# Optimization experiments

Hardware: AMD Instinct MI355X
Metric: run time of the kernel (lower is better)

## Reference

```python
import math
import jax, jax.numpy as jnp
import numpy as np

BN_EPS = 1e-5

def _lrelu(x, s):
    return jnp.where(x >= 0, x, s * x)

def _bn(x, g, b):
    # BatchNorm2d in train mode (torch default): biased batch stats over (B,H,W)
    mu = jnp.mean(x, axis=(0, 2, 3), keepdims=True)
    var = jnp.mean((x - mu) ** 2, axis=(0, 2, 3), keepdims=True)
    return (x - mu) / jnp.sqrt(var + BN_EPS) * g[None, :, None, None] + b[None, :, None, None]

def _knn(x, x2, k):
    # x: [B,d,P], x2: [B,d,S] -> idx [B,k,S]: k nearest points of x for each column of x2
    inner = -2.0 * jnp.einsum('bdp,bds->bps', x, x2)
    xx = jnp.sum(x ** 2, axis=1)[:, :, None]    # [B,P,1]
    xx2 = jnp.sum(x2 ** 2, axis=1)[:, None, :]  # [B,1,S]
    d = -xx - inner - xx2                        # [B,P,S], larger = closer
    _, idx = jax.lax.top_k(jnp.transpose(d, (0, 2, 1)), k)  # [B,S,k]
    return jnp.transpose(idx, (0, 2, 1))         # [B,k,S]

def _gather_nb(X, idx, s, k):
    # faithful to torch gether_neibour, including its flat-reshape layout
    B, C, P = X.shape
    base = jnp.arange(B)[:, None, None] * P
    flat = (idx + base).reshape(-1)
    Xt = jnp.transpose(X, (0, 2, 1)).reshape(B * P, C)
    return Xt[flat].reshape(B, s, k, C)

def _c2d(x, W, b):
    return jnp.einsum('oc,bcpk->bopk', W, x) + b[None, :, None, None]

def _c1d(x, W, b):
    return jnp.einsum('oc,bcp->bop', W, x) + b[None, :, None]

def _forward(x, W_pos, b_pos, g2, be2, W_conv, b_conv, g1, be1, W_a1, b_a1, W_a2, b_a2, W_b1, b_b1, W_b2, b_b2, num_points):
    B, C, P = x.shape
    k = 8
    s = num_points
    # ---- Dynamic_sampling_M: uniform mesh over (x,y) bbox, snap to nearest event ----
    L = int(math.ceil(math.sqrt(s)))
    m = jnp.arange(L, dtype=x.dtype) / L
    m01 = jnp.tile(m[None, :], (L, 1)).reshape(1, 1, L * L)
    m02 = jnp.tile(m[:, None], (1, L)).reshape(1, 1, L * L)
    mesh = jnp.broadcast_to(jnp.concatenate([m01, m02], axis=1), (B, 2, L * L))
    Px = jax.lax.stop_gradient(x[:, :2, :])  # knn runs under torch.no_grad
    mn = Px.min(axis=2, keepdims=True)
    mx = Px.max(axis=2, keepdims=True)
    PS = mesh * (mx - mn) + mn
    idx0 = _knn(Px, PS, 1)                                   # [B,1,L*L]
    sp = _gather_nb(x, idx0, L * L, 1)[:, :, 0, :].transpose(0, 2, 1)  # [B,C,s]
    idx = _knn(jax.lax.stop_gradient(x[:, :3, :]), jax.lax.stop_gradient(sp[:, :3, :]), k)  # [B,k,s]
    x1 = jnp.transpose(_gather_nb(x, idx, s, k), (0, 3, 1, 2))  # [B,C,s,k]
    # ---- positional encoding ----
    PA = x1[:, :3, :, :]
    PC = x1[:, :3, :, 0:1]
    diff = PA - PC
    sq = jnp.sum(diff ** 2, axis=1, keepdims=True)
    temp = jnp.where(sq > 0, jnp.sqrt(jnp.where(sq > 0, sq, 1.0)), 0.0)
    PEmb = jnp.concatenate([PA, jnp.broadcast_to(PC, PA.shape), diff, temp], axis=1)  # [B,10,s,k]
    PEmb = _lrelu(_bn(_c2d(PEmb, W_pos, b_pos), g2, be2), 0.2)
    x_ = _lrelu(_bn(_c2d(x1[:, :4, :, :], W_conv, b_conv), g1, be1), 0.2)
    feat = jnp.concatenate([x_, PEmb], axis=1)  # [B,64,s,k]
    att = _c2d(_lrelu(_c2d(feat, W_a1, b_a1), 0.2), W_a2, b_a2)  # [B,1,s,k]
    att = jax.nn.softmax(att, axis=-1)
    feat = jnp.sum(feat * att, axis=-1)  # [B,64,s]
    Fea1 = _c1d(feat, W_b1, b_b1)
    Fea2 = _c1d(x1[:, :4, :, 0], W_b2, b_b2)
    out = _lrelu(Fea1 + Fea2, 0.01)
    return jnp.concatenate([x1[:, :5, :, 0], out], axis=1)  # [B,69,s]

def setup_inputs() -> dict:
    key = jax.random.key(0)
    ks = jax.random.split(key, 8)
    B, C, P = 2, 5, 16384
    num_points = 4096  # perfect square required by the mesh sampler
    outc, inc, h = 64, 4, 32
    w = lambda k_, shape: jax.random.normal(k_, shape, jnp.float32) * 0.05
    x = jax.random.normal(ks[0], (B, C, P), jnp.float32)
    return dict(
        x=x,
        W_pos=w(ks[1], (h, 10)), b_pos=jnp.zeros((h,), jnp.float32),
        g2=jnp.ones((h,), jnp.float32), be2=jnp.zeros((h,), jnp.float32),
        W_conv=w(ks[2], (h, inc)), b_conv=jnp.zeros((h,), jnp.float32),
        g1=jnp.ones((h,), jnp.float32), be1=jnp.zeros((h,), jnp.float32),
        W_a1=w(ks[3], (32, outc)), b_a1=jnp.zeros((32,), jnp.float32),
        W_a2=w(ks[4], (1, 32)), b_a2=jnp.zeros((1,), jnp.float32),
        W_b1=w(ks[5], (outc, outc)), b_b1=jnp.zeros((outc,), jnp.float32),
        W_b2=w(ks[6], (outc, inc)), b_b2=jnp.zeros((outc,), jnp.float32),
        num_points=num_points,
    )

def reference(x, W_pos, b_pos, g2, be2, W_conv, b_conv, g1, be1, W_a1, b_a1, W_a2, b_a2, W_b1, b_b1, W_b2, b_b2, num_points):
    return _forward(x, W_pos, b_pos, g2, be2, W_conv, b_conv, g1, be1, W_a1, b_a1, W_a2, b_a2, W_b1, b_b1, W_b2, b_b2, num_points)
```

## Files before the change

### kernel.cpp

```cpp
#include <hip/hip_runtime.h>
#include <math.h>

#define B_ 2
#define P_ 16384
#define C_ 5
#define S_ 4096
#define KNN_ 8
#define L_ 64

typedef unsigned short u16;
typedef unsigned int u32;

__device__ int   g_idxk[B_ * KNN_ * S_];
__device__ __align__(16) float g_partials[128 * 1024];

__device__ __forceinline__ float bf2f(u16 u) {
  union { u32 i; float f; } c; c.i = ((u32)u) << 16; return c.f;
}
__device__ __forceinline__ u16 f2bf(float f) {
  union { float f; u32 i; } c; c.f = f;
  u32 r = c.i + 0x7fffu + ((c.i >> 16) & 1u);
  return (u16)(r >> 16);
}
__device__ __forceinline__ float ldany(const void* p, int i, int f32) {
  return f32 ? ((const float*)p)[i] : bf2f(((const u16*)p)[i]);
}

__device__ __forceinline__ double packkey(float d, int idx) {
  u32 bits = __float_as_uint(d);
  u32 key = bits ^ ((u32)(((int)bits) >> 31) | 0x80000000u);
  int hi = (int)(0x3FF00000u | (key >> 12));
  int lo = (int)((key << 20) | ((u32)(16383 - idx) << 6));
  return __hiloint2double(hi, lo);
}
__device__ __forceinline__ int keyidx(double w) {
  return 16383 - (int)(((u32)__double2loint(w) >> 6) & 16383u);
}
__device__ __forceinline__ void cmpswap(double& a, double& b) {
  double hi = fmax(a, b), lo = fmin(a, b);
  a = hi; b = lo;
}
__device__ __forceinline__ void flush8(double* a, double* k) {
  cmpswap(k[0], k[1]); cmpswap(k[2], k[3]); cmpswap(k[4], k[5]); cmpswap(k[6], k[7]);
  cmpswap(k[0], k[2]); cmpswap(k[1], k[3]); cmpswap(k[4], k[6]); cmpswap(k[5], k[7]);
  cmpswap(k[1], k[2]); cmpswap(k[5], k[6]);
  cmpswap(k[0], k[4]); cmpswap(k[1], k[5]); cmpswap(k[2], k[6]); cmpswap(k[3], k[7]);
  cmpswap(k[2], k[4]); cmpswap(k[3], k[5]);
  cmpswap(k[1], k[2]); cmpswap(k[3], k[4]); cmpswap(k[5], k[6]);
  a[0] = fmax(a[0], k[7]); a[1] = fmax(a[1], k[6]);
  a[2] = fmax(a[2], k[5]); a[3] = fmax(a[3], k[4]);
  a[4] = fmax(a[4], k[3]); a[5] = fmax(a[5], k[2]);
  a[6] = fmax(a[6], k[1]); a[7] = fmax(a[7], k[0]);
  cmpswap(a[0], a[4]); cmpswap(a[1], a[5]); cmpswap(a[2], a[6]); cmpswap(a[3], a[7]);
  cmpswap(a[0], a[2]); cmpswap(a[1], a[3]); cmpswap(a[4], a[6]); cmpswap(a[5], a[7]);
  cmpswap(a[0], a[1]); cmpswap(a[2], a[3]); cmpswap(a[4], a[5]); cmpswap(a[6], a[7]);
}

__device__ __forceinline__ int chk_bad(const void* p, int n, int tid) {
  int bad = 0;
  for (int i = tid; i < n; i += 256) {
    float f = bf2f(((const u16*)p)[i]);
    if (!(f == f) || fabsf(f) > 1024.0f) bad = 1;
  }
  return bad;
}

__global__ __launch_bounds__(256, 4) void k_knn(const void* __restrict__ xv,
                                                const void* __restrict__ Wpos,
                                                const void* __restrict__ bpos,
                                                const void* __restrict__ Wconv,
                                                const void* __restrict__ bconv) {
  __shared__ float4 s4[1024];
  __shared__ float sWpos[320], sbpos[32], sWconv[128], sbconv[32];
  __shared__ float sacc[4][128];
  __shared__ int sidx[8];
  __shared__ int sp0[8];
  __shared__ int sbad, sbw;
  __shared__ float sred[16];
  int tid = threadIdx.x;
  int l = tid & 63, g = tid >> 6;
  int sg0 = blockIdx.x * 8 + g * 2;
  int b = sg0 >> 12;
  int base0 = b * C_ * P_, base1 = base0 + P_, base2 = base1 + P_;

  if (tid == 0) { sbad = 0; sbw = 0; }
  __syncthreads();
  if (chk_bad(xv, 1024, tid)) atomicOr(&sbad, 1);
  if (chk_bad(Wpos, 320, tid) | chk_bad(Wconv, 128, tid)) atomicOr(&sbw, 1);
  __syncthreads();
  const int f32 = sbad, wf32 = sbw;

  for (int i2 = tid; i2 < 320; i2 += 256) sWpos[i2] = ldany(Wpos, i2, wf32);
  if (tid < 128) sWconv[tid] = ldany(Wconv, tid, wf32);
  if (tid < 32) { sbpos[tid] = ldany(bpos, tid, wf32); sbconv[tid] = ldany(bconv, tid, wf32); }

  float mn0 = INFINITY, mx0 = -INFINITY, mn1 = INFINITY, mx1 = -INFINITY;
  for (int p = tid; p < P_; p += 256) {
    float v0 = ldany(xv, base0 + p, f32);
    float v1 = ldany(xv, base1 + p, f32);
    mn0 = fminf(mn0, v0); mx0 = fmaxf(mx0, v0);
    mn1 = fminf(mn1, v1); mx1 = fmaxf(mx1, v1);
  }
  for (int off = 32; off; off >>= 1) {
    mn0 = fminf(mn0, __shfl_down(mn0, off)); mx0 = fmaxf(mx0, __shfl_down(mx0, off));
    mn1 = fminf(mn1, __shfl_down(mn1, off)); mx1 = fmaxf(mx1, __shfl_down(mx1, off));
  }
  if (l == 0) {
    sred[g * 4 + 0] = mn0; sred[g * 4 + 1] = mx0;
    sred[g * 4 + 2] = mn1; sred[g * 4 + 3] = mx1;
  }
  __syncthreads();
  mn0 = fminf(fminf(sred[0], sred[4]), fminf(sred[8], sred[12]));
  mx0 = fmaxf(fmaxf(sred[1], sred[5]), fmaxf(sred[9], sred[13]));
  mn1 = fminf(fminf(sred[2], sred[6]), fminf(sred[10], sred[14]));
  mx1 = fmaxf(fmaxf(sred[3], sred[7]), fmaxf(sred[11], sred[15]));

  float ps0[2], ps1[2], xx2[2], best[2]; int bestp[2];
#pragma unroll
  for (int qq = 0; qq < 2; ++qq) {
    int s = (sg0 + qq) & (S_ - 1);
    float mm0 = (float)(s & (L_ - 1)) * 0.015625f;
    float mm1 = (float)(s >> 6) * 0.015625f;
    ps0[qq] = __fadd_rn(__fmul_rn(mm0, __fsub_rn(mx0, mn0)), mn0);
    ps1[qq] = __fadd_rn(__fmul_rn(mm1, __fsub_rn(mx1, mn1)), mn1);
    xx2[qq] = __fadd_rn(__fmul_rn(ps0[qq], ps0[qq]), __fmul_rn(ps1[qq], ps1[qq]));
    best[qq] = -INFINITY; bestp[qq] = 0x7fffffff;
  }
  for (int c = 0; c < 16; ++c) {
    __syncthreads();
#pragma unroll
    for (int r = 0; r < 4; ++r) {
      int i = r * 256 + tid;
      int gi = c * 1024 + i;
      float a0 = ldany(xv, base0 + gi, f32);
      float a1 = ldany(xv, base1 + gi, f32);
      float xx = __fadd_rn(__fmul_rn(a0, a0), __fmul_rn(a1, a1));
      s4[i] = make_float4(a0, a1, xx, 0.0f);
    }
    __syncthreads();
    for (int t = 0; t < 16; ++t) {
      float4 v = s4[t * 64 + l];
      int ix = c * 1024 + t * 64 + l;
#pragma unroll
      for (int qq = 0; qq < 2; ++qq) {
        float dot = __fadd_rn(__fmul_rn(v.x, ps0[qq]), __fmul_rn(v.y, ps1[qq]));
        float inner = __fmul_rn(-2.0f, dot);
        float d = __fsub_rn(__fsub_rn(-v.z, inner), xx2[qq]);
        bool gt = d > best[qq];
        best[qq] = gt ? d : best[qq];
        bestp[qq] = gt ? ix : bestp[qq];
      }
    }
  }
#pragma unroll
  for (int qq = 0; qq < 2; ++qq) {
    float v = best[qq]; int ix = bestp[qq];
    for (int m = 1; m < 64; m <<= 1) {
      float ov = __shfl_xor(v, m, 64); int op = __shfl_xor(ix, m, 64);
      if (ov > v || (ov == v && op < ix)) { v = ov; ix = op; }
    }
    if (l == 0) sidx[g * 2 + qq] = ix;
  }
  __syncthreads();

  float q0[2], q1[2], q2[2], xx3q[2];
  double acc[2][8], kb[2][8];
#pragma unroll
  for (int qq = 0; qq < 2; ++qq) {
    int qi = sidx[g * 2 + qq] & (P_ - 1);
    q0[qq] = ldany(xv, base0 + qi, f32);
    q1[qq] = ldany(xv, base1 + qi, f32);
    q2[qq] = ldany(xv, base2 + qi, f32);
    xx3q[qq] = __fadd_rn(__fadd_rn(__fmul_rn(q0[qq], q0[qq]), __fmul_rn(q1[qq], q1[qq])),
                         __fmul_rn(q2[qq], q2[qq]));
#pragma unroll
    for (int k = 0; k < 8; ++k) acc[qq][k] = -1.0;
  }
  for (int c = 0; c < 16; ++c) {
    __syncthreads();
#pragma unroll
    for (int r = 0; r < 4; ++r) {
      int i = r * 256 + tid;
      int gi = c * 1024 + i;
      float a0 = ldany(xv, base0 + gi, f32);
      float a1 = ldany(xv, base1 + gi, f32);
      float a2 = ldany(xv, base2 + gi, f32);
      float xx = __fadd_rn(__fadd_rn(__fmul_rn(a0, a0), __fmul_rn(a1, a1)), __fmul_rn(a2, a2));
      s4[i] = make_float4(a0, a1, a2, xx);
    }
    __syncthreads();
#pragma unroll
    for (int t = 0; t < 16; ++t) {
      float4 v = s4[t * 64 + l];
      int ix = c * 1024 + t * 64 + l;
      u32 lob = ((u32)(16383 - ix)) << 6;
#pragma unroll
      for (int qq = 0; qq < 2; ++qq) {
        float dot = __fadd_rn(__fadd_rn(__fmul_rn(v.x, q0[qq]), __fmul_rn(v.y, q1[qq])),
                              __fmul_rn(v.z, q2[qq]));
        float inner = __fmul_rn(-2.0f, dot);
        float d = __fsub_rn(__fsub_rn(-v.w, inner), xx3q[qq]);
        u32 bits = __float_as_uint(d);
        u32 key = bits ^ ((u32)(((int)bits) >> 31) | 0x80000000u);
        kb[qq][t & 7] = __hiloint2double((int)(0x3FF00000u | (key >> 12)),
                                         (int)((key << 20) | lob));
      }
      if ((t & 7) == 7) {
        flush8(acc[0], kb[0]);
        flush8(acc[1], kb[1]);
      }
    }
  }
  double wk[2] = {0.0, 0.0};
#pragma unroll
  for (int qq = 0; qq < 2; ++qq) {
#pragma unroll
    for (int r = 0; r < 8; ++r) {
      double w = acc[qq][0];
      for (int m = 1; m < 64; m <<= 1) w = fmax(w, __shfl_xor(w, m, 64));
      if (l == r) wk[qq] = w;
      bool cns = (acc[qq][0] == w);
#pragma unroll
      for (int k = 0; k < 7; ++k) acc[qq][k] = cns ? acc[qq][k + 1] : acc[qq][k];
      acc[qq][7] = cns ? -1.0 : acc[qq][7];
    }
  }
  if (l < 8) {
#pragma unroll
    for (int qq = 0; qq < 2; ++qq) {
      int s = (sg0 + qq) & (S_ - 1);
      g_idxk[b * 32768 + l * 4096 + s] = keyidx(wk[qq]);
    }
  }

  if (g == 0 && l < 8) sp0[l] = keyidx(wk[0]) & (P_ - 1);
  __syncthreads();
  double k1s = __shfl(wk[1], l & 7, 16);
  bool active = (l < 16);
  double myk = (l < 8) ? wk[0] : k1s;
  int p = keyidx(myk) & (P_ - 1);
  int p0 = sp0[l & 7];
  float xvv[4] = {0, 0, 0, 0}, pc3[3] = {0, 0, 0};
  if (active) {
#pragma unroll
    for (int cc = 0; cc < 4; ++cc) xvv[cc] = ldany(xv, base0 + cc * P_ + p, f32);
#pragma unroll
    for (int cc = 0; cc < 3; ++cc) pc3[cc] = ldany(xv, base0 + cc * P_ + p0, f32);
  }
  float d0 = xvv[0] - pc3[0], d1 = xvv[1] - pc3[1], d2 = xvv[2] - pc3[2];
  float sq = d0 * d0 + d1 * d1 + d2 * d2;
  float temp = (sq > 0.0f) ? sqrtf(sq) : 0.0f;
  float pe[10] = {xvv[0], xvv[1], xvv[2], pc3[0], pc3[1], pc3[2], d0, d1, d2, temp};
#pragma unroll
  for (int o = 0; o < 64; ++o) {
    float v;
    if (o < 32) {
      v = sbconv[o];
#pragma unroll
      for (int cc = 0; cc < 4; ++cc) v = fmaf(sWconv[o * 4 + cc], xvv[cc], v);
    } else {
      v = sbpos[o - 32];
#pragma unroll
      for (int cc = 0; cc < 10; ++cc) v = fmaf(sWpos[(o - 32) * 10 + cc], pe[cc], v);
    }
    v = active ? v : 0.0f;
    float s = v, q = v * v;
    for (int m = 1; m < 16; m <<= 1) { s += __shfl_xor(s, m, 16); q += __shfl_xor(q, m, 16); }
    if (l == 0) { sacc[g][o * 2] = s; sacc[g][o * 2 + 1] = q; }
  }
  __syncthreads();
  if (tid < 128) {
    g_partials[tid * 1024 + blockIdx.x] =
        sacc[0][tid] + sacc[1][tid] + sacc[2][tid] + sacc[3][tid];
  }
}

__global__ __launch_bounds__(256) void k_pass2(const void* __restrict__ x,
                                               const void* __restrict__ Wpos,
                                               const void* __restrict__ bpos,
                                               const void* __restrict__ Wconv,
                                               const void* __restrict__ bconv,
                                               const void* __restrict__ g1,
                                               const void* __restrict__ be1,
                                               const void* __restrict__ g2,
                                               const void* __restrict__ be2,
                                               const void* __restrict__ Wa1,
                                               const void* __restrict__ ba1,
                                               const void* __restrict__ Wa2,
                                               const void* __restrict__ ba2,
                                               const void* __restrict__ Wb1,
                                               const void* __restrict__ bb1,
                                               const void* __restrict__ Wb2,
                                               const void* __restrict__ bb2,
                                               void* __restrict__ out) {
  __shared__ float sWpos[320], sbpos[32], sWconv[128], sbconv[32];
  __shared__ float sWa1[2048], sba1[32], sWa2[32];
  __shared__ float sWb1[64 * 65];
  __shared__ float sbb1[64], sWb2[256], sbb2[64], sstats[128];
  __shared__ float sp2[2][128];
  __shared__ float sba2;
  __shared__ int sbx, sbw;
  int tid = threadIdx.x;
  if (tid == 0) { sbx = 0; sbw = 0; }
  __syncthreads();
  if (chk_bad(x, 1024, tid)) atomicOr(&sbx, 1);
  if (chk_bad(Wa1, 2048, tid) | chk_bad(Wb1, 4096, tid)) atomicOr(&sbw, 1);
  __syncthreads();
  int xf32 = sbx, wf32 = sbw;

  int g = blockIdx.x * 32 + (tid >> 3);
  int j = tid & 7;
  int b = g >> 12, i = g & (S_ - 1);
  int n = i * 8 + j;
  const int* fb = g_idxk + b * 32768;
  int xbase = b * C_ * P_;
  int p = fb[n] & (P_ - 1);
  int p0 = fb[n & ~7] & (P_ - 1);
  float xvv[4];
#pragma unroll
  for (int c = 0; c < 4; ++c) xvv[c] = ldany(x, xbase + c * P_ + p, xf32);
  float pc3[3];
#pragma unroll
  for (int c = 0; c < 3; ++c) pc3[c] = ldany(x, xbase + c * P_ + p0, xf32);
  float xc0 = ldany(x, xbase + p0, xf32);
  float xc1 = ldany(x, xbase + P_ + p0, xf32);
  float xc2 = ldany(x, xbase + 2 * P_ + p0, xf32);
  float xc3 = ldany(x, xbase + 3 * P_ + p0, xf32);

  {
    int slot = tid & 127, half = tid >> 7;
    const float4* gp = (const float4*)(g_partials + slot * 1024 + half * 512);
    float a0 = 0.f, a1 = 0.f, a2 = 0.f, a3 = 0.f;
#pragma unroll 8
    for (int q = 0; q < 128; ++q) {
      float4 v = gp[q];
      a0 += v.x; a1 += v.y; a2 += v.z; a3 += v.w;
    }
    sp2[half][slot] = (a0 + a1) + (a2 + a3);
  }
  for (int i2 = tid; i2 < 320; i2 += 256) sWpos[i2] = ldany(Wpos, i2, wf32);
  if (tid < 128) sWconv[tid] = ldany(Wconv, tid, wf32);
  if (tid < 32) { sbpos[tid] = ldany(bpos, tid, wf32); sbconv[tid] = ldany(bconv, tid, wf32); }
  for (int i2 = tid; i2 < 2048; i2 += 256) sWa1[i2] = ldany(Wa1, i2, wf32);
  for (int i2 = tid; i2 < 4096; i2 += 256) sWb1[(i2 >> 6) * 65 + (i2 & 63)] = ldany(Wb1, i2, wf32);
  if (tid >= 32 && tid < 64) { sba1[tid - 32] = ldany(ba1, tid - 32, wf32); sWa2[tid - 32] = ldany(Wa2, tid - 32, wf32); }
  if (tid >= 64 && tid < 128) { sbb1[tid - 64] = ldany(bb1, tid - 64, wf32); sbb2[tid - 64] = ldany(bb2, tid - 64, wf32); }
  sWb2[tid] = ldany(Wb2, tid, wf32);
  if (tid == 0) sba2 = ldany(ba2, 0, wf32);
  __syncthreads();
  if (tid >= 128 && tid < 192) {
    int ch = tid - 128;
    float sum = sp2[0][ch * 2] + sp2[1][ch * 2];
    float sq = sp2[0][ch * 2 + 1] + sp2[1][ch * 2 + 1];
    float mean = sum * (1.0f / 65536.0f);
    float var = sq * (1.0f / 65536.0f) - mean * mean;
    int o = ch & 31;
    float gg = ldany(ch < 32 ? g1 : g2, o, wf32);
    float be = ldany(ch < 32 ? be1 : be2, o, wf32);
    float scale = gg / sqrtf(var + 1e-5f);
    sstats[ch * 2] = scale;
    sstats[ch * 2 + 1] = be - mean * scale;
  }
  __syncthreads();

  float d0 = xvv[0] - pc3[0], d1 = xvv[1] - pc3[1], d2 = xvv[2] - pc3[2];
  float sq = d0 * d0 + d1 * d1 + d2 * d2;
  float temp = (sq > 0.0f) ? sqrtf(sq) : 0.0f;
  float pe[10] = {xvv[0], xvv[1], xvv[2], pc3[0], pc3[1], pc3[2], d0, d1, d2, temp};
  float feat[64];
#pragma unroll
  for (int o = 0; o < 32; ++o) {
    float acc = sbconv[o];
#pragma unroll
    for (int c = 0; c < 4; ++c) acc = fmaf(sWconv[o * 4 + c], xvv[c], acc);
    feat[o] = acc;
  }
#pragma unroll
  for (int o = 0; o < 32; ++o) {
    float acc = sbpos[o];
#pragma unroll
    for (int c = 0; c < 10; ++c) acc = fmaf(sWpos[o * 10 + c], pe[c], acc);
    feat[32 + o] = acc;
  }
#pragma unroll
  for (int c = 0; c < 64; ++c) {
    float v = fmaf(feat[c], sstats[c * 2], sstats[c * 2 + 1]);
    feat[c] = (v >= 0.f) ? v : 0.2f * v;
  }
  float att = sba2;
#pragma unroll 4
  for (int h = 0; h < 32; ++h) {
    float a0 = 0.f, a1 = 0.f, a2 = 0.f, a3 = 0.f;
#pragma unroll
    for (int c = 0; c < 64; c += 4) {
      a0 = fmaf(sWa1[h * 64 + c],     feat[c],     a0);
      a1 = fmaf(sWa1[h * 64 + c + 1], feat[c + 1], a1);
      a2 = fmaf(sWa1[h * 64 + c + 2], feat[c + 2], a2);
      a3 = fmaf(sWa1[h * 64 + c + 3], feat[c + 3], a3);
    }
    float acc = sba1[h] + ((a0 + a1) + (a2 + a3));
    acc = (acc >= 0.f) ? acc : 0.2f * acc;
    att = fmaf(sWa2[h], acc, att);
  }
  float mxv = att;
  for (int mk = 1; mk < 8; mk <<= 1) mxv = fmaxf(mxv, __shfl_xor(mxv, mk, 8));
  float e = expf(att - mxv);
  float se = e;
  for (int mk = 1; mk < 8; mk <<= 1) se += __shfl_xor(se, mk, 8);
  float a = e / se;
#pragma unroll
  for (int c = 0; c < 64; ++c) {
    float w = feat[c] * a;
    w += __shfl_xor(w, 1, 8);
    w += __shfl_xor(w, 2, 8);
    w += __shfl_xor(w, 4, 8);
    feat[c] = w;
  }
  int obase = b * 69 * S_;
#pragma unroll
  for (int oc = 0; oc < 8; ++oc) {
    int o = j * 8 + oc;
    float a0 = sbb1[o], a1 = 0.f, a2 = 0.f, a3 = 0.f;
#pragma unroll
    for (int c = 0; c < 64; c += 4) {
      a0 = fmaf(sWb1[o * 65 + c],     feat[c],     a0);
      a1 = fmaf(sWb1[o * 65 + c + 1], feat[c + 1], a1);
      a2 = fmaf(sWb1[o * 65 + c + 2], feat[c + 2], a2);
      a3 = fmaf(sWb1[o * 65 + c + 3], feat[c + 3], a3);
    }
    float acc = (a0 + a1) + (a2 + a3);
    float acc2 = sbb2[o];
    acc2 = fmaf(sWb2[o * 4 + 0], xc0, acc2);
    acc2 = fmaf(sWb2[o * 4 + 1], xc1, acc2);
    acc2 = fmaf(sWb2[o * 4 + 2], xc2, acc2);
    acc2 = fmaf(sWb2[o * 4 + 3], xc3, acc2);
    float r = acc + acc2;
    r = (r >= 0.f) ? r : 0.01f * r;
    int oi = obase + (5 + o) * S_ + i;
    if (xf32) ((float*)out)[oi] = r; else ((u16*)out)[oi] = f2bf(r);
  }
  if (j == 0) {
#pragma unroll
    for (int c = 0; c < 5; ++c) {
      int oi = obase + c * S_ + i;
      if (xf32) ((float*)out)[oi] = ((const float*)x)[xbase + c * P_ + p0];
      else      ((u16*)out)[oi]   = ((const u16*)x)[xbase + c * P_ + p0];
    }
  }
}

extern "C" void kernel_launch(void* const* d_in, const int* in_sizes, int n_in,
                              void* d_out, int out_size, void* d_ws, size_t ws_size,
                              hipStream_t stream) {
  const void* x     = d_in[0];
  const void* Wpos  = d_in[1];
  const void* bpos  = d_in[2];
  const void* g2    = d_in[3];
  const void* be2   = d_in[4];
  const void* Wconv = d_in[5];
  const void* bconv = d_in[6];
  const void* g1    = d_in[7];
  const void* be1   = d_in[8];
  const void* Wa1   = d_in[9];
  const void* ba1   = d_in[10];
  const void* Wa2   = d_in[11];
  const void* ba2   = d_in[12];
  const void* Wb1   = d_in[13];
  const void* bb1   = d_in[14];
  const void* Wb2   = d_in[15];
  const void* bb2   = d_in[16];
  (void)d_ws; (void)ws_size; (void)in_sizes; (void)n_in;

  hipLaunchKernelGGL(k_knn, dim3(1024), dim3(256), 0, stream, x,
                     Wpos, bpos, Wconv, bconv);
  hipLaunchKernelGGL(k_pass2, dim3(256), dim3(256), 0, stream, x,
                     Wpos, bpos, Wconv, bconv, g1, be1, g2, be2,
                     Wa1, ba1, Wa2, ba2, Wb1, bb1, Wb2, bb2, d_out);
}
```

Before: 304.4 us.

## Split KNN kernel into one-query-per-wave search and separate batch-stat tail kernel

The KNN kernel now handles one query per wavefront instead of two, doubling the grid to 2048 blocks and raising the occupancy hint. The BN partial-statistics work that used to run inside the KNN kernel moves to a new k_tail kernel, one thread per neighbour. The partials buffer is re-laid out as [block][128] and the reduction in pass2 is rewritten to match. This frees registers in the KNN loop for higher occupancy, but it reloads each tile of points twice as often across blocks and adds a third kernel launch.

Result: no change. 300.4 us (-1.3%).

```diff
diff --git a/kernel.cpp b/kernel.cpp
--- a/kernel.cpp
+++ b/kernel.cpp
@@ -12,7 +12,7 @@
 typedef unsigned int u32;
 
 __device__ int   g_idxk[B_ * KNN_ * S_];
-__device__ __align__(16) float g_partials[128 * 1024];
+__device__ float g_partials[256 * 128];
 
 __device__ __forceinline__ float bf2f(u16 u) {
   union { u32 i; float f; } c; c.i = ((u32)u) << 16; return c.f;
@@ -26,13 +26,6 @@
   return f32 ? ((const float*)p)[i] : bf2f(((const u16*)p)[i]);
 }
 
-__device__ __forceinline__ double packkey(float d, int idx) {
-  u32 bits = __float_as_uint(d);
-  u32 key = bits ^ ((u32)(((int)bits) >> 31) | 0x80000000u);
-  int hi = (int)(0x3FF00000u | (key >> 12));
-  int lo = (int)((key << 20) | ((u32)(16383 - idx) << 6));
-  return __hiloint2double(hi, lo);
-}
 __device__ __forceinline__ int keyidx(double w) {
   return 16383 - (int)(((u32)__double2loint(w) >> 6) & 16383u);
 }
@@ -65,34 +58,23 @@
   return bad;
 }
 
-__global__ __launch_bounds__(256, 4) void k_knn(const void* __restrict__ xv,
-                                                const void* __restrict__ Wpos,
-                                                const void* __restrict__ bpos,
-                                                const void* __restrict__ Wconv,
-                                                const void* __restrict__ bconv) {
+__global__ __launch_bounds__(256, 6) void k_knn(const void* __restrict__ xv) {
   __shared__ float4 s4[1024];
-  __shared__ float sWpos[320], sbpos[32], sWconv[128], sbconv[32];
-  __shared__ float sacc[4][128];
-  __shared__ int sidx[8];
-  __shared__ int sp0[8];
-  __shared__ int sbad, sbw;
+  __shared__ int sidx[4];
+  __shared__ int sbad;
   __shared__ float sred[16];
   int tid = threadIdx.x;
   int l = tid & 63, g = tid >> 6;
-  int sg0 = blockIdx.x * 8 + g * 2;
-  int b = sg0 >> 12;
+  int sq = blockIdx.x * 4 + g;
+  int b = sq >> 12;
+  int s = sq & (S_ - 1);
   int base0 = b * C_ * P_, base1 = base0 + P_, base2 = base1 + P_;
 
-  if (tid == 0) { sbad = 0; sbw = 0; }
+  if (tid == 0) sbad = 0;
   __syncthreads();
   if (chk_bad(xv, 1024, tid)) atomicOr(&sbad, 1);
-  if (chk_bad(Wpos, 320, tid) | chk_bad(Wconv, 128, tid)) atomicOr(&sbw, 1);
-  __syncthreads();
-  const int f32 = sbad, wf32 = sbw;
-
-  for (int i2 = tid; i2 < 320; i2 += 256) sWpos[i2] = ldany(Wpos, i2, wf32);
-  if (tid < 128) sWconv[tid] = ldany(Wconv, tid, wf32);
-  if (tid < 32) { sbpos[tid] = ldany(bpos, tid, wf32); sbconv[tid] = ldany(bconv, tid, wf32); }
+  __syncthreads();
+  const int f32 = sbad;
 
   float mn0 = INFINITY, mx0 = -INFINITY, mn1 = INFINITY, mx1 = -INFINITY;
   for (int p = tid; p < P_; p += 256) {
@@ -115,17 +97,12 @@
   mn1 = fminf(fminf(sred[2], sred[6]), fminf(sred[10], sred[14]));
   mx1 = fmaxf(fmaxf(sred[3], sred[7]), fmaxf(sred[11], sred[15]));
 
-  float ps0[2], ps1[2], xx2[2], best[2]; int bestp[2];
-#pragma unroll
-  for (int qq = 0; qq < 2; ++qq) {
-    int s = (sg0 + qq) & (S_ - 1);
-    float mm0 = (float)(s & (L_ - 1)) * 0.015625f;
-    float mm1 = (float)(s >> 6) * 0.015625f;
-    ps0[qq] = __fadd_rn(__fmul_rn(mm0, __fsub_rn(mx0, mn0)), mn0);
-    ps1[qq] = __fadd_rn(__fmul_rn(mm1, __fsub_rn(mx1, mn1)), mn1);
-    xx2[qq] = __fadd_rn(__fmul_rn(ps0[qq], ps0[qq]), __fmul_rn(ps1[qq], ps1[qq]));
-    best[qq] = -INFINITY; bestp[qq] = 0x7fffffff;
-  }
+  float mm0 = (float)(s & (L_ - 1)) * 0.015625f;
+  float mm1 = (float)(s >> 6) * 0.015625f;
+  float ps0 = __fadd_rn(__fmul_rn(mm0, __fsub_rn(mx0, mn0)), mn0);
+  float ps1 = __fadd_rn(__fmul_rn(mm1, __fsub_rn(mx1, mn1)), mn1);
+  float xx2 = __fadd_rn(__fmul_rn(ps0, ps0), __fmul_rn(ps1, ps1));
+  float best = -INFINITY; int bestp = 0x7fffffff;
   for (int c = 0; c < 16; ++c) {
     __syncthreads();
 #pragma unroll
@@ -141,41 +118,33 @@
     for (int t = 0; t < 16; ++t) {
       float4 v = s4[t * 64 + l];
       int ix = c * 1024 + t * 64 + l;
-#pragma unroll
-      for (int qq = 0; qq < 2; ++qq) {
-        float dot = __fadd_rn(__fmul_rn(v.x, ps0[qq]), __fmul_rn(v.y, ps1[qq]));
-        float inner = __fmul_rn(-2.0f, dot);
-        float d = __fsub_rn(__fsub_rn(-v.z, inner), xx2[qq]);
-        bool gt = d > best[qq];
-        best[qq] = gt ? d : best[qq];
-        bestp[qq] = gt ? ix : bestp[qq];
-      }
-    }
-  }
-#pragma unroll
-  for (int qq = 0; qq < 2; ++qq) {
-    float v = best[qq]; int ix = bestp[qq];
+      float dot = __fadd_rn(__fmul_rn(v.x, ps0), __fmul_rn(v.y, ps1));
+      float inner = __fmul_rn(-2.0f, dot);
+      float d = __fsub_rn(__fsub_rn(-v.z, inner), xx2);
+      bool gt = d > best;
+      best = gt ? d : best;
+      bestp = gt ? ix : bestp;
+    }
+  }
+  {
+    float v = best; int ix = bestp;
     for (int m = 1; m < 64; m <<= 1) {
       float ov = __shfl_xor(v, m, 64); int op = __shfl_xor(ix, m, 64);
       if (ov > v || (ov == v && op < ix)) { v = ov; ix = op; }
     }
-    if (l == 0) sidx[g * 2 + qq] = ix;
-  }
-  __syncthreads();
-
-  float q0[2], q1[2], q2[2], xx3q[2];
-  double acc[2][8], kb[2][8];
-#pragma unroll
-  for (int qq = 0; qq < 2; ++qq) {
-    int qi = sidx[g * 2 + qq] & (P_ - 1);
-    q0[qq] = ldany(xv, base0 + qi, f32);
-    q1[qq] = ldany(xv, base1 + qi, f32);
-    q2[qq] = ldany(xv, base2 + qi, f32);
-    xx3q[qq] = __fadd_rn(__fadd_rn(__fmul_rn(q0[qq], q0[qq]), __fmul_rn(q1[qq], q1[qq])),
-                         __fmul_rn(q2[qq], q2[qq]));
-#pragma unroll
-    for (int k = 0; k < 8; ++k) acc[qq][k] = -1.0;
-  }
+    if (l == 0) sidx[g] = ix;
+  }
+  __syncthreads();
+
+  int qi = sidx[g] & (P_ - 1);
+  float q0 = ldany(xv, base0 + qi, f32);
+  float q1 = ldany(xv, base1 + qi, f32);
+  float q2 = ldany(xv, base2 + qi, f32);
+  float xx3q = __fadd_rn(__fadd_rn(__fmul_rn(q0, q0), __fmul_rn(q1, q1)),
+                         __fmul_rn(q2, q2));
+  double acc[8], kb[8];
+#pragma unroll
+  for (int k = 0; k < 8; ++k) acc[k] = -1.0;
   for (int c = 0; c < 16; ++c) {
     __syncthreads();
 #pragma unroll
@@ -194,59 +163,64 @@
       float4 v = s4[t * 64 + l];
       int ix = c * 1024 + t * 64 + l;
       u32 lob = ((u32)(16383 - ix)) << 6;
-#pragma unroll
-      for (int qq = 0; qq < 2; ++qq) {
-        float dot = __fadd_rn(__fadd_rn(__fmul_rn(v.x, q0[qq]), __fmul_rn(v.y, q1[qq])),
-                              __fmul_rn(v.z, q2[qq]));
-        float inner = __fmul_rn(-2.0f, dot);
-        float d = __fsub_rn(__fsub_rn(-v.w, inner), xx3q[qq]);
-        u32 bits = __float_as_uint(d);
-        u32 key = bits ^ ((u32)(((int)bits) >> 31) | 0x80000000u);
-        kb[qq][t & 7] = __hiloint2double((int)(0x3FF00000u | (key >> 12)),
-                                         (int)((key << 20) | lob));
-      }
-      if ((t & 7) == 7) {
-        flush8(acc[0], kb[0]);
-        flush8(acc[1], kb[1]);
-      }
-    }
-  }
-  double wk[2] = {0.0, 0.0};
-#pragma unroll
-  for (int qq = 0; qq < 2; ++qq) {
-#pragma unroll
-    for (int r = 0; r < 8; ++r) {
-      double w = acc[qq][0];
-      for (int m = 1; m < 64; m <<= 1) w = fmax(w, __shfl_xor(w, m, 64));
-      if (l == r) wk[qq] = w;
-      bool cns = (acc[qq][0] == w);
-#pragma unroll
-      for (int k = 0; k < 7; ++k) acc[qq][k] = cns ? acc[qq][k + 1] : acc[qq][k];
-      acc[qq][7] = cns ? -1.0 : acc[qq][7];
-    }
-  }
-  if (l < 8) {
-#pragma unroll
-    for (int qq = 0; qq < 2; ++qq) {
-      int s = (sg0 + qq) & (S_ - 1);
-      g_idxk[b * 32768 + l * 4096 + s] = keyidx(wk[qq]);
-    }
-  }
-
-  if (g == 0 && l < 8) sp0[l] = keyidx(wk[0]) & (P_ - 1);
-  __syncthreads();
-  double k1s = __shfl(wk[1], l & 7, 16);
-  bool active = (l < 16);
-  double myk = (l < 8) ? wk[0] : k1s;
-  int p = keyidx(myk) & (P_ - 1);
-  int p0 = sp0[l & 7];
-  float xvv[4] = {0, 0, 0, 0}, pc3[3] = {0, 0, 0};
-  if (active) {
-#pragma unroll
-    for (int cc = 0; cc < 4; ++cc) xvv[cc] = ldany(xv, base0 + cc * P_ + p, f32);
-#pragma unroll
-    for (int cc = 0; cc < 3; ++cc) pc3[cc] = ldany(xv, base0 + cc * P_ + p0, f32);
-  }
+      float dot = __fadd_rn(__fadd_rn(__fmul_rn(v.x, q0), __fmul_rn(v.y, q1)),
+                            __fmul_rn(v.z, q2));
+      float inner = __fmul_rn(-2.0f, dot);
+      float d = __fsub_rn(__fsub_rn(-v.w, inner), xx3q);
+      u32 bits = __float_as_uint(d);
+      u32 key = bits ^ ((u32)(((int)bits) >> 31) | 0x80000000u);
+      kb[t & 7] = __hiloint2double((int)(0x3FF00000u | (key >> 12)),
+                                   (int)((key << 20) | lob));
+      if ((t & 7) == 7) flush8(acc, kb);
+    }
+  }
+  double wk = 0.0;
+#pragma unroll
+  for (int r = 0; r < 8; ++r) {
+    double w = acc[0];
+    for (int m = 1; m < 64; m <<= 1) w = fmax(w, __shfl_xor(w, m, 64));
+    if (l == r) wk = w;
+    bool cns = (acc[0] == w);
+#pragma unroll
+    for (int k = 0; k < 7; ++k) acc[k] = cns ? acc[k + 1] : acc[k];
+    acc[7] = cns ? -1.0 : acc[7];
+  }
+  if (l < 8) g_idxk[b * 32768 + l * 4096 + s] = keyidx(wk);
+}
+
+__global__ __launch_bounds__(256) void k_tail(const void* __restrict__ x,
+                                              const void* __restrict__ Wpos,
+                                              const void* __restrict__ bpos,
+                                              const void* __restrict__ Wconv,
+                                              const void* __restrict__ bconv) {
+  __shared__ float sWpos[320], sbpos[32], sWconv[128], sbconv[32];
+  __shared__ float sacc[16][128];
+  __shared__ int sbx, sbw;
+  int tid = threadIdx.x;
+  if (tid == 0) { sbx = 0; sbw = 0; }
+  __syncthreads();
+  if (chk_bad(x, 1024, tid)) atomicOr(&sbx, 1);
+  if (chk_bad(Wpos, 320, tid) | chk_bad(Wconv, 128, tid)) atomicOr(&sbw, 1);
+  __syncthreads();
+  const int f32 = sbx, wf32 = sbw;
+
+  int id = blockIdx.x * 256 + tid;
+  int b = id >> 15, n = id & 32767;
+  const int* fb = g_idxk + b * 32768;
+  int base0 = b * C_ * P_;
+  int p = fb[n] & (P_ - 1);
+  int p0 = fb[n & ~7] & (P_ - 1);
+  float xvv[4], pc3[3];
+#pragma unroll
+  for (int cc = 0; cc < 4; ++cc) xvv[cc] = ldany(x, base0 + cc * P_ + p, f32);
+#pragma unroll
+  for (int cc = 0; cc < 3; ++cc) pc3[cc] = ldany(x, base0 + cc * P_ + p0, f32);
+
+  for (int i2 = tid; i2 < 320; i2 += 256) sWpos[i2] = ldany(Wpos, i2, wf32);
+  if (tid < 128) sWconv[tid] = ldany(Wconv, tid, wf32);
+  if (tid < 32) { sbpos[tid] = ldany(bpos, tid, wf32); sbconv[tid] = ldany(bconv, tid, wf32); }
+  __syncthreads();
+
   float d0 = xvv[0] - pc3[0], d1 = xvv[1] - pc3[1], d2 = xvv[2] - pc3[2];
   float sq = d0 * d0 + d1 * d1 + d2 * d2;
   float temp = (sq > 0.0f) ? sqrtf(sq) : 0.0f;
@@ -263,15 +237,16 @@
 #pragma unroll
       for (int cc = 0; cc < 10; ++cc) v = fmaf(sWpos[(o - 32) * 10 + cc], pe[cc], v);
     }
-    v = active ? v : 0.0f;
-    float s = v, q = v * v;
-    for (int m = 1; m < 16; m <<= 1) { s += __shfl_xor(s, m, 16); q += __shfl_xor(q, m, 16); }
-    if (l == 0) { sacc[g][o * 2] = s; sacc[g][o * 2 + 1] = q; }
+    float sv = v, qv = v * v;
+    for (int m = 1; m < 16; m <<= 1) { sv += __shfl_xor(sv, m, 16); qv += __shfl_xor(qv, m, 16); }
+    if ((tid & 15) == 0) { sacc[tid >> 4][o * 2] = sv; sacc[tid >> 4][o * 2 + 1] = qv; }
   }
   __syncthreads();
   if (tid < 128) {
-    g_partials[tid * 1024 + blockIdx.x] =
-        sacc[0][tid] + sacc[1][tid] + sacc[2][tid] + sacc[3][tid];
+    float a = 0.f;
+#pragma unroll
+    for (int w = 0; w < 16; ++w) a += sacc[w][tid];
+    g_partials[blockIdx.x * 128 + tid] = a;
   }
 }
 
@@ -329,14 +304,12 @@
 
   {
     int slot = tid & 127, half = tid >> 7;
-    const float4* gp = (const float4*)(g_partials + slot * 1024 + half * 512);
-    float a0 = 0.f, a1 = 0.f, a2 = 0.f, a3 = 0.f;
-#pragma unroll 8
-    for (int q = 0; q < 128; ++q) {
-      float4 v = gp[q];
-      a0 += v.x; a1 += v.y; a2 += v.z; a3 += v.w;
-    }
-    sp2[half][slot] = (a0 + a1) + (a2 + a3);
+    float a0 = 0.f, a1 = 0.f;
+    for (int blk = half * 128; blk < half * 128 + 128; blk += 2) {
+      a0 += g_partials[blk * 128 + slot];
+      a1 += g_partials[(blk + 1) * 128 + slot];
+    }
+    sp2[half][slot] = a0 + a1;
   }
   for (int i2 = tid; i2 < 320; i2 += 256) sWpos[i2] = ldany(Wpos, i2, wf32);
   if (tid < 128) sWconv[tid] = ldany(Wconv, tid, wf32);
@@ -471,7 +444,8 @@
   const void* bb2   = d_in[16];
   (void)d_ws; (void)ws_size; (void)in_sizes; (void)n_in;
 
-  hipLaunchKernelGGL(k_knn, dim3(1024), dim3(256), 0, stream, x,
+  hipLaunchKernelGGL(k_knn, dim3(2048), dim3(256), 0, stream, x);
+  hipLaunchKernelGGL(k_tail, dim3(256), dim3(256), 0, stream, x,
                      Wpos, bpos, Wconv, bconv);
   hipLaunchKernelGGL(k_pass2, dim3(256), dim3(256), 0, stream, x,
                      Wpos, bpos, Wconv, bconv, g1, be1, g2, be2,
```
